# Kernel optimization log

Hardware: AMD Instinct MI355X
Metric: run time of the kernel (lower is better)

The kernel has to match this reference:

```python
import jax, jax.numpy as jnp
import numpy as np

B = 128          # graphs
NPG = 512        # nodes per graph
N = B * NPG      # total nodes
DEG = 8
E = N * DEG      # total edges (intra-graph)
D = 100          # num_feature_dim / num_node_labels
HID = 128        # config.hidden
HEADS = 8
F1 = 20          # per-head dim of first GATConv in each GATNet
RATIO = 0.5
K = int(np.ceil(RATIO * NPG))  # nodes kept per graph by SAGPooling
NEG_SLOPE = 0.2


def setup_inputs() -> dict:
    key = jax.random.key(0)
    ks = jax.random.split(key, 24)
    x = jax.random.randint(ks[0], (N,), 0, D)
    # intra-graph random edges: local ids in [0, NPG) + graph offset
    src_l = jax.random.randint(ks[1], (B, NPG * DEG), 0, NPG)
    dst_l = jax.random.randint(ks[2], (B, NPG * DEG), 0, NPG)
    off = (jnp.arange(B) * NPG)[:, None]
    edge_index = jnp.stack([(src_l + off).ravel(), (dst_l + off).ravel()])
    batch = jnp.repeat(jnp.arange(B), NPG)

    def lin(k, fan_in, fan_out):
        return jax.random.normal(k, (fan_in, fan_out), jnp.float32) / np.sqrt(fan_in)

    def att(k, h, f):
        return jax.random.normal(k, (h, f), jnp.float32) * 0.1

    p = {
        # GATNet A (conv1): GATConv(D, 20, heads=8) then GATConv(160, HID, heads=1)
        "W_a1": lin(ks[3], D, HEADS * F1), "asrc_a1": att(ks[4], HEADS, F1),
        "adst_a1": att(ks[5], HEADS, F1), "b_a1": jnp.zeros((HEADS * F1,), jnp.float32),
        "W_a2": lin(ks[6], HEADS * F1, HID), "asrc_a2": att(ks[7], 1, HID),
        "adst_a2": att(ks[8], 1, HID), "b_a2": jnp.zeros((HID,), jnp.float32),
        # GATNet B (conv4): GATConv(HID, 20, heads=8) then GATConv(160, HID, heads=1)
        "W_b1": lin(ks[9], HID, HEADS * F1), "asrc_b1": att(ks[10], HEADS, F1),
        "adst_b1": att(ks[11], HEADS, F1), "b_b1": jnp.zeros((HEADS * F1,), jnp.float32),
        "W_b2": lin(ks[12], HEADS * F1, HID), "asrc_b2": att(ks[13], 1, HID),
        "adst_b2": att(ks[14], 1, HID), "b_b2": jnp.zeros((HID,), jnp.float32),
        # SAGPooling GraphConv(HID, 1)
        "w_rel": lin(ks[15], HID, 1), "w_root": lin(ks[16], HID, 1),
        "b_pool": jnp.zeros((1,), jnp.float32),
    }
    return {"x": x, "edge_index": edge_index, "batch": batch, **p}


def _gat_conv(h, src, dst, W, asrc, adst, b):
    """PyG GATConv (with self-loops already included in src/dst)."""
    Hh, Ff = asrc.shape
    z = (h @ W).reshape(N, Hh, Ff)                       # [N,H,F]
    es = jnp.sum(z * asrc, axis=-1)                      # [N,H] source logits
    ed = jnp.sum(z * adst, axis=-1)                      # [N,H] dest logits
    e = jax.nn.leaky_relu(es[src] + ed[dst], NEG_SLOPE)  # [E',H]
    m = jax.ops.segment_max(e, dst, num_segments=N)
    m = jnp.where(jnp.isfinite(m), m, 0.0)
    ex = jnp.exp(e - m[dst])
    den = jax.ops.segment_sum(ex, dst, num_segments=N)
    alpha = ex / (den[dst] + 1e-16)
    out = jax.ops.segment_sum(z[src] * alpha[:, :, None], dst, num_segments=N)
    return out.reshape(N, Hh * Ff) + b


def reference(x, edge_index, batch,
              W_a1, asrc_a1, adst_a1, b_a1, W_a2, asrc_a2, adst_a2, b_a2,
              W_b1, asrc_b1, adst_b1, b_b1, W_b2, asrc_b2, adst_b2, b_b2,
              w_rel, w_root, b_pool):
    src, dst = edge_index[0], edge_index[1]
    loops = jnp.arange(N)
    src_sl = jnp.concatenate([src, loops])  # GATConv adds self loops
    dst_sl = jnp.concatenate([dst, loops])

    h = jax.nn.one_hot(x, D, dtype=jnp.float32)
    # GATNet A: conv1 -> relu -> conv2 ; outer relu (dropout is eval no-op)
    h = jax.nn.relu(_gat_conv(h, src_sl, dst_sl, W_a1, asrc_a1, adst_a1, b_a1))
    h = _gat_conv(h, src_sl, dst_sl, W_a2, asrc_a2, adst_a2, b_a2)
    h = jax.nn.relu(h)
    # GATNet B
    h = jax.nn.relu(_gat_conv(h, src_sl, dst_sl, W_b1, asrc_b1, adst_b1, b_b1))
    h = _gat_conv(h, src_sl, dst_sl, W_b2, asrc_b2, adst_b2, b_b2)
    h = jax.nn.relu(h)

    # SAGPooling: GraphConv(HID,1) score (no self loops), tanh, per-graph top-k
    nbr = jax.ops.segment_sum(h[src], dst, num_segments=N)
    score = jnp.tanh(nbr @ w_rel + h @ w_root + b_pool).ravel()   # [N]
    sv, si = jax.lax.top_k(score.reshape(B, NPG), K)              # [B,K]
    perm = (si + (jnp.arange(B) * NPG)[:, None]).ravel()          # global node ids
    x_sel = h[perm] * sv.ravel()[:, None]                         # [B*K, HID]
    pooled = jnp.max(x_sel.reshape(B, K, HID), axis=1)            # global_max_pool
    batch_out = jnp.repeat(jnp.arange(B), K)
    return (pooled, perm, sv.ravel(), batch_out)
```

## Files before the change

kernel.cpp:

```cpp
#include <hip/hip_runtime.h>
#include <math.h>

#define N_NODES 65536
#define NPG     512
#define NGRAPH  128
#define E_EDGES 524288
#define MAXDEG  64
#define NHEADS  8
#define F1      20
#define HID     128
#define D160    160
#define KSEL    256
#define NLBL    100

#define IMG_A2_ELEMS (144*168)
#define IMG_B1_ELEMS (176*136)
#define PB_ZERO 0
#define PB_A2   64
#define PB_B1   (PB_A2 + 95)
#define PB_B2   (PB_B1 + 94)
#define PB_WA1  (PB_B2 + 95)
#define PB_EST  (PB_WA1 + 63)
#define PB_TOT  (PB_EST + 7)

typedef unsigned short ushort_t;
typedef unsigned int   uint_t;
typedef unsigned long long u64;
typedef __attribute__((ext_vector_type(8))) short short8;
typedef __attribute__((ext_vector_type(4))) float f32x4;

__device__ __forceinline__ float lrelu(float x){ return x > 0.f ? x : 0.2f*x; }
__device__ __forceinline__ ushort_t f2bf(float f){
    uint_t u = __float_as_uint(f);
    return (ushort_t)((u + 0x7FFFu + ((u >> 16) & 1u)) >> 16);
}
__device__ __forceinline__ float bf2f(ushort_t u){ return __uint_as_float(((uint_t)u) << 16); }
__device__ __forceinline__ float bflo(uint_t v){ return __uint_as_float(v << 16); }
__device__ __forceinline__ float bfhi(uint_t v){ return __uint_as_float(v & 0xFFFF0000u); }
__device__ __forceinline__ int xswz(int bid, int nblocks){
    return (bid & 7) * (nblocks >> 3) + (bid >> 3);
}

__device__ __forceinline__ u64 comp_make(float s, int idx){
    uint_t u = __float_as_uint(s);
    u ^= (u & 0x80000000u) ? 0xFFFFFFFFu : 0x80000000u;
    return ((u64)u << 32) | (u64)(511 - idx);
}
__device__ __forceinline__ float comp_score(u64 c){
    uint_t u = (uint_t)(c >> 32);
    u ^= (u & 0x80000000u) ? 0x80000000u : 0xFFFFFFFFu;
    return __uint_as_float(u);
}
__device__ __forceinline__ int comp_idx(u64 c){ return 511 - (int)(c & 0x1FFu); }
__device__ __forceinline__ u64 shfl_xor_u64(u64 x, int m){
    uint_t lo = __shfl_xor((uint_t)x, m);
    uint_t hi = __shfl_xor((uint_t)(x >> 32), m);
    return ((u64)hi << 32) | lo;
}

__global__ void k_prep(const float* __restrict__ Wa1, const float* __restrict__ as1,
                       const float* __restrict__ ad1,
                       const float* __restrict__ Wa2, const float* __restrict__ as2,
                       const float* __restrict__ ad2,
                       const float* __restrict__ Wb1, const float* __restrict__ asb1,
                       const float* __restrict__ adb1,
                       const float* __restrict__ Wb2, const float* __restrict__ asb2,
                       const float* __restrict__ adb2,
                       int* __restrict__ deg,
                       ushort_t* __restrict__ imgA2, ushort_t* __restrict__ imgB1,
                       ushort_t* __restrict__ imgB2,
                       ushort_t* __restrict__ Wbf, float* __restrict__ esT,
                       float* __restrict__ edT){
    int bid = blockIdx.x, tid = threadIdx.x;
    if(bid < PB_A2){
        ((uint4*)deg)[(bid - PB_ZERO)*256 + tid] = (uint4){0,0,0,0};
    } else if(bid < PB_B1 || (bid >= PB_B2 && bid < PB_WA1)){
        bool isB2 = (bid >= PB_B2);
        int j = (bid - (isB2 ? PB_B2 : PB_A2))*256 + tid;
        if(j < IMG_A2_ELEMS){
            const float* W  = isB2 ? Wb2 : Wa2;
            const float* as = isB2 ? asb2 : as2;
            const float* ad = isB2 ? adb2 : ad2;
            int n = j / 168, k = j - n*168;
            float v = 0.f;
            if(k < 160){
                if(n < 128) v = W[k*128 + n];
                else if(n < 130){
                    const float* av = (n == 128) ? as : ad;
                    float s = 0.f;
                    for(int c=0; c<128; ++c) s += W[k*128 + c]*av[c];
                    v = s;
                }
            }
            (isB2 ? imgB2 : imgA2)[j] = f2bf(v);
        }
    } else if(bid < PB_B2){
        int j = (bid - PB_B1)*256 + tid;
        if(j < IMG_B1_ELEMS){
            int n = j / 136, k = j - n*136;
            float v = 0.f;
            if(k < 128){
                if(n < 160) v = Wb1[k*160 + n];
                else {
                    int j2 = n - 160, h = j2 & 7;
                    const float* av = ((j2 < 8) ? asb1 : adb1) + h*F1;
                    const float* wr = Wb1 + k*160 + h*F1;
                    float s = 0.f;
                    #pragma unroll
                    for(int f=0; f<F1; ++f) s += wr[f]*av[f];
                    v = s;
                }
            }
            imgB1[j] = f2bf(v);
        }
    } else if(bid < PB_EST){
        int j = (bid - PB_WA1)*256 + tid;
        if(j < NLBL*D160) Wbf[j] = f2bf(Wa1[j]);
    } else {
        int t = (bid - PB_EST)*256 + tid;
        if(t < NLBL*16){
            int lbl = t >> 4, j = t & 15, h = j & 7;
            const float* av = ((j < 8) ? as1 : ad1) + h*F1;
            const float* wr = Wa1 + lbl*D160 + h*F1;
            float s = 0.f;
            #pragma unroll
            for(int f=0; f<F1; ++f) s += wr[f]*av[f];
            if(j < 8) esT[lbl*8 + h] = s;
            else      edT[lbl*8 + h] = s;
        }
    }
}

__global__ void k_build_ell(const int* __restrict__ src, const int* __restrict__ dst,
                            int* __restrict__ deg, int* __restrict__ ell){
    int blk = xswz(blockIdx.x, E_EDGES/256);
    int e = blk*blockDim.x + threadIdx.x;
    int d = dst[e];
    int p = atomicAdd(&deg[d], 1);
    if(p < MAXDEG) ell[d*MAXDEG + p] = src[e];
}

__global__ __launch_bounds__(256) void k_attn8_a(const int* __restrict__ x,
        const int* __restrict__ deg, const int* __restrict__ ell,
        const ushort_t* __restrict__ Wbf, const float* __restrict__ esT,
        const float* __restrict__ edT, const float* __restrict__ bias,
        ushort_t* __restrict__ out){
    __shared__ __align__(16) ushort_t Wl[NLBL*D160];
    __shared__ float esL[NLBL*8], edL[NLBL*8];
    int tid = threadIdx.x;
    for(int i = tid; i < NLBL*D160/8; i += 256)
        ((uint4*)Wl)[i] = ((const uint4*)Wbf)[i];
    for(int i = tid; i < NLBL*8; i += 256){ esL[i] = esT[i]; edL[i] = edT[i]; }
    __syncthreads();
    int blk = xswz(blockIdx.x, N_NODES*NHEADS/256);
    int t = blk*256 + tid;
    int n = t >> 3, h = t & 7;
    int dg = deg[n]; if(dg > MAXDEG) dg = MAXDEG;
    int lbl = x[n];
    float edn = edL[lbl*8 + h];
    float wself = expf(lrelu(esL[lbl*8 + h] + edn));
    float den = wself;
    float acc[F1];
    {
        const uint_t* zn = (const uint_t*)Wl + lbl*80 + h*10;
        #pragma unroll
        for(int f=0; f<10; ++f){
            uint_t v = zn[f];
            acc[2*f]   = wself*bflo(v);
            acc[2*f+1] = wself*bfhi(v);
        }
    }
    const int* el = ell + n*MAXDEG;
    int i = 0;
    for(; i+2 <= dg; i += 2){
        int sa = el[i], sb = el[i+1];
        int la = x[sa], lb = x[sb];
        float wa = expf(lrelu(esL[la*8 + h] + edn));
        float wb = expf(lrelu(esL[lb*8 + h] + edn));
        den += wa + wb;
        const uint_t* za = (const uint_t*)Wl + la*80 + h*10;
        const uint_t* zb = (const uint_t*)Wl + lb*80 + h*10;
        #pragma unroll
        for(int f=0; f<10; ++f){
            uint_t va = za[f], vb = zb[f];
            acc[2*f]   += wa*bflo(va) + wb*bflo(vb);
            acc[2*f+1] += wa*bfhi(va) + wb*bfhi(vb);
        }
    }
    if(i < dg){
        int sa = el[i];
        int la = x[sa];
        float wa = expf(lrelu(esL[la*8 + h] + edn));
        den += wa;
        const uint_t* za = (const uint_t*)Wl + la*80 + h*10;
        #pragma unroll
        for(int f=0; f<10; ++f){
            uint_t va = za[f];
            acc[2*f]   += wa*bflo(va);
            acc[2*f+1] += wa*bfhi(va);
        }
    }
    float inv = 1.f/(den + 1e-16f);
    uint_t* o = (uint_t*)(out + (size_t)n*D160 + h*F1);
    const float* bb = bias + h*F1;
    #pragma unroll
    for(int f=0; f<10; ++f){
        float v0 = fmaxf(acc[2*f]*inv   + bb[2*f],   0.f);
        float v1 = fmaxf(acc[2*f+1]*inv + bb[2*f+1], 0.f);
        o[f] = (uint_t)f2bf(v0) | ((uint_t)f2bf(v1) << 16);
    }
}

__global__ __launch_bounds__(512) void k_attn8b(const int* __restrict__ deg,
        const int* __restrict__ ell, const ushort_t* __restrict__ z8,
        const float* __restrict__ es8, const float* __restrict__ ed8,
        const float* __restrict__ bias, ushort_t* __restrict__ out){
    __shared__ __align__(16) ushort_t zl[512*88];
    __shared__ __align__(16) float4 esl[512];
    __shared__ __align__(16) float4 edl[512];
    int tid = threadIdx.x;
    int blk = xswz(blockIdx.x, NGRAPH*2);
    int g = blk >> 1, hg = blk & 1;
    int base = g*NPG;
    for(int idx = tid; idx < 512*10; idx += 512){
        int row = idx/10, q = idx - (idx/10)*10;
        uint4 v = *(const uint4*)(z8 + (size_t)(base+row)*D160 + hg*80 + q*8);
        *(uint4*)(zl + row*88 + q*8) = v;
    }
    esl[tid] = *(const float4*)(es8 + (size_t)(base+tid)*8 + hg*4);
    edl[tid] = *(const float4*)(ed8 + (size_t)(base+tid)*8 + hg*4);
    __syncthreads();
    int n = tid;
    int dg = deg[base+n]; if(dg > MAXDEG) dg = MAXDEG;
    const int* el = ell + (size_t)(base+n)*MAXDEG;
    float4 edn = edl[n];
    float4 esn = esl[n];
    float w0 = expf(lrelu(esn.x + edn.x));
    float w1 = expf(lrelu(esn.y + edn.y));
    float w2 = expf(lrelu(esn.z + edn.z));
    float w3 = expf(lrelu(esn.w + edn.w));
    float den0 = w0, den1 = w1, den2 = w2, den3 = w3;
    float acc[80];
    #pragma unroll
    for(int q=0; q<10; ++q){
        uint4 v = *(const uint4*)(zl + n*88 + q*8);
        const uint_t* vu = (const uint_t*)&v;
        #pragma unroll
        for(int r=0; r<4; ++r){
            int ch = q*8 + r*2;
            float wA = (ch < 20) ? w0 : (ch < 40) ? w1 : (ch < 60) ? w2 : w3;
            float wB = (ch+1 < 20) ? w0 : (ch+1 < 40) ? w1 : (ch+1 < 60) ? w2 : w3;
            acc[ch]   = wA*bflo(vu[r]);
            acc[ch+1] = wB*bfhi(vu[r]);
        }
    }
    for(int i=0; i<dg; ++i){
        int s = el[i] & (NPG-1);
        float4 es_s = esl[s];
        float wa0 = expf(lrelu(es_s.x + edn.x));
        float wa1 = expf(lrelu(es_s.y + edn.y));
        float wa2 = expf(lrelu(es_s.z + edn.z));
        float wa3 = expf(lrelu(es_s.w + edn.w));
        den0 += wa0; den1 += wa1; den2 += wa2; den3 += wa3;
        #pragma unroll
        for(int q=0; q<10; ++q){
            uint4 v = *(const uint4*)(zl + s*88 + q*8);
            const uint_t* vu = (const uint_t*)&v;
            #pragma unroll
            for(int r=0; r<4; ++r){
                int ch = q*8 + r*2;
                float wA = (ch < 20) ? wa0 : (ch < 40) ? wa1 : (ch < 60) ? wa2 : wa3;
                float wB = (ch+1 < 20) ? wa0 : (ch+1 < 40) ? wa1 : (ch+1 < 60) ? wa2 : wa3;
                acc[ch]   += wA*bflo(vu[r]);
                acc[ch+1] += wB*bfhi(vu[r]);
            }
        }
    }
    float inv0 = 1.f/(den0 + 1e-16f);
    float inv1 = 1.f/(den1 + 1e-16f);
    float inv2 = 1.f/(den2 + 1e-16f);
    float inv3 = 1.f/(den3 + 1e-16f);
    const float* bb = bias + hg*80;
    uint_t* o = (uint_t*)out + (size_t)(base+n)*80 + hg*40;
    #pragma unroll
    for(int q=0; q<10; ++q){
        #pragma unroll
        for(int r=0; r<4; ++r){
            int ch = q*8 + r*2;
            float iA = (ch < 20) ? inv0 : (ch < 40) ? inv1 : (ch < 60) ? inv2 : inv3;
            float iB = (ch+1 < 20) ? inv0 : (ch+1 < 40) ? inv1 : (ch+1 < 60) ? inv2 : inv3;
            float v0 = fmaxf(acc[ch]*iA   + bb[ch],   0.f);
            float v1 = fmaxf(acc[ch+1]*iB + bb[ch+1], 0.f);
            o[q*4 + r] = (uint_t)f2bf(v0) | ((uint_t)f2bf(v1) << 16);
        }
    }
}

template<int IN, int OUTC, int OUTIMG, bool ESED8>
__global__ __launch_bounds__(256) void k_gemm2(const ushort_t* __restrict__ Wimg,
                                               const ushort_t* __restrict__ A,
                                               ushort_t* __restrict__ C,
                                               float* __restrict__ oa,
                                               float* __restrict__ ob){
    constexpr int LDW = IN + 8;
    constexpr int NT = OUTIMG/16;
    constexpr int NC = OUTC/16;
    constexpr int KS = IN/32;
    constexpr int ELEMS = OUTIMG*LDW;
    __shared__ __align__(16) ushort_t Wt[ELEMS];
    int tid = threadIdx.x;
    int blk = xswz(blockIdx.x, N_NODES/64);
    int wave = tid >> 6, lane = tid & 63;
    int col16 = lane & 15;
    int kq = (lane >> 4) * 8;
    int row = blk*64 + wave*16 + col16;
    const ushort_t* Ar = A + (size_t)row*IN + kq;
    short8 afr[KS];
    #pragma unroll
    for(int ks=0; ks<KS; ++ks)
        afr[ks] = *reinterpret_cast<const short8*>(Ar + ks*32);
    for(int i = tid; i < ELEMS/8; i += 256)
        ((uint4*)Wt)[i] = ((const uint4*)Wimg)[i];
    __syncthreads();
    f32x4 acc[NT];
    #pragma unroll
    for(int c=0;c<NT;++c) acc[c] = (f32x4){0.f,0.f,0.f,0.f};
    #pragma unroll
    for(int ks=0; ks<KS; ++ks){
        #pragma unroll
        for(int c=0;c<NT;++c){
            short8 bf = *reinterpret_cast<const short8*>(&Wt[(c*16 + col16)*LDW + ks*32 + kq]);
            acc[c] = __builtin_amdgcn_mfma_f32_16x16x32_bf16(afr[ks], bf, acc[c], 0, 0, 0);
        }
    }
    int rbase = blk*64 + wave*16 + (lane >> 4)*4;
    #pragma unroll
    for(int c=0;c<NC;++c){
        #pragma unroll
        for(int r=0;r<4;++r){
            C[(size_t)(rbase + r)*OUTC + c*16 + col16] = f2bf(acc[c][r]);
        }
    }
    if(ESED8){
        #pragma unroll
        for(int r=0;r<4;++r){
            float v = acc[NT-1][r];
            if(col16 < 8) oa[(size_t)(rbase + r)*8 + col16] = v;
            else          ob[(size_t)(rbase + r)*8 + (col16 - 8)] = v;
        }
    } else {
        if(col16 == 0){
            #pragma unroll
            for(int r=0;r<4;++r) oa[rbase + r] = acc[NT-1][r];
        }
        if(col16 == 1){
            #pragma unroll
            for(int r=0;r<4;++r) ob[rbase + r] = acc[NT-1][r];
        }
    }
}

template<bool DOT>
__global__ void k_attn1v(const int* __restrict__ deg, const int* __restrict__ ell,
                         const ushort_t* __restrict__ Z, const float* __restrict__ es,
                         const float* __restrict__ ed, const float* __restrict__ bias,
                         ushort_t* __restrict__ out,
                         const float* __restrict__ wa, const float* __restrict__ wb,
                         float* __restrict__ oa, float* __restrict__ ob){
    int blk = xswz(blockIdx.x, N_NODES*4/256);
    int t = blk*256 + threadIdx.x;
    int n = t >> 2, qt = t & 3;
    int dg = deg[n]; if(dg > MAXDEG) dg = MAXDEG;
    float edn = ed[n];
    float wself = expf(lrelu(es[n] + edn));
    float den = wself;
    const uint4* Zu = (const uint4*)Z;
    float acc[32];
    {
        const uint4* zr = Zu + (size_t)n*16 + qt*4;
        uint4 vs[4];
        #pragma unroll
        for(int q=0;q<4;++q) vs[q] = zr[q];
        #pragma unroll
        for(int q=0;q<4;++q){
            const uint_t* vu = (const uint_t*)&vs[q];
            #pragma unroll
            for(int r=0;r<4;++r){
                acc[q*8+r*2]   = wself*bflo(vu[r]);
                acc[q*8+r*2+1] = wself*bfhi(vu[r]);
            }
        }
    }
    const int* el = ell + (size_t)n*MAXDEG;
    int i = 0;
    for(; i+2 <= dg; i += 2){
        int sa = el[i], sb = el[i+1];
        float ea = es[sa], eb = es[sb];
        const uint4* za = Zu + (size_t)sa*16 + qt*4;
        const uint4* zb = Zu + (size_t)sb*16 + qt*4;
        uint4 va[4], vb4[4];
        #pragma unroll
        for(int q=0;q<4;++q){ va[q] = za[q]; vb4[q] = zb[q]; }
        float wA = expf(lrelu(ea + edn));
        float wB = expf(lrelu(eb + edn));
        den += wA + wB;
        #pragma unroll
        for(int q=0;q<4;++q){
            const uint_t* au = (const uint_t*)&va[q];
            const uint_t* bu = (const uint_t*)&vb4[q];
            #pragma unroll
            for(int r=0;r<4;++r){
                acc[q*8+r*2]   += wA*bflo(au[r]) + wB*bflo(bu[r]);
                acc[q*8+r*2+1] += wA*bfhi(au[r]) + wB*bfhi(bu[r]);
            }
        }
    }
    if(i < dg){
        int sa = el[i];
        float ea = es[sa];
        const uint4* za = Zu + (size_t)sa*16 + qt*4;
        uint4 va[4];
        #pragma unroll
        for(int q=0;q<4;++q) va[q] = za[q];
        float wA = expf(lrelu(ea + edn));
        den += wA;
        #pragma unroll
        for(int q=0;q<4;++q){
            const uint_t* au = (const uint_t*)&va[q];
            #pragma unroll
            for(int r=0;r<4;++r){
                acc[q*8+r*2]   += wA*bflo(au[r]);
                acc[q*8+r*2+1] += wA*bfhi(au[r]);
            }
        }
    }
    float inv = 1.f/(den + 1e-16f);
    const float* bb = bias + qt*32;
    float pa = 0.f, pb = 0.f;
    uint_t* o = (uint_t*)out + (size_t)n*64 + qt*16;
    #pragma unroll
    for(int q=0;q<4;++q){
        uint4 w;
        uint_t* wu = (uint_t*)&w;
        #pragma unroll
        for(int r=0;r<4;++r){
            int ch = q*8 + r*2;
            float r0 = fmaxf(acc[ch]*inv   + bb[ch],   0.f);
            float r1 = fmaxf(acc[ch+1]*inv + bb[ch+1], 0.f);
            wu[r] = (uint_t)f2bf(r0) | ((uint_t)f2bf(r1) << 16);
            if(DOT){
                pa += r0*wa[qt*32 + ch] + r1*wa[qt*32 + ch + 1];
                pb += r0*wb[qt*32 + ch] + r1*wb[qt*32 + ch + 1];
            }
        }
        *(uint4*)(o + q*4) = w;
    }
    if(DOT){
        pa += __shfl_xor(pa, 1); pa += __shfl_xor(pa, 2);
        pb += __shfl_xor(pb, 1); pb += __shfl_xor(pb, 2);
        if(qt == 0){ oa[n] = pa; ob[n] = pb; }
    }
}

__global__ void k_score(const int* __restrict__ deg, const int* __restrict__ ell,
                        const float* __restrict__ yrel, const float* __restrict__ rroot,
                        const float* __restrict__ bpool, float* __restrict__ score){
    int blk = xswz(blockIdx.x, N_NODES/256);
    int n = blk*blockDim.x + threadIdx.x;
    int dg = deg[n]; if(dg > MAXDEG) dg = MAXDEG;
    float s = rroot[n] + bpool[0];
    const int* el = ell + n*MAXDEG;
    int i = 0;
    for(; i+4 <= dg; i += 4){
        float y0 = yrel[el[i]],   y1 = yrel[el[i+1]];
        float y2 = yrel[el[i+2]], y3 = yrel[el[i+3]];
        s += (y0 + y1) + (y2 + y3);
    }
    for(; i < dg; ++i) s += yrel[el[i]];
    score[n] = tanhf(s);
}

__global__ __launch_bounds__(512) void k_topk_pool(const float* __restrict__ score,
                                                   const ushort_t* __restrict__ H,
                                                   float* __restrict__ pooled,
                                                   float* __restrict__ perm_f,
                                                   float* __restrict__ sv,
                                                   float* __restrict__ batch_f){
    __shared__ int   sidx[KSEL];
    __shared__ float sval[KSEL];
    __shared__ float pmax[512];
    int g = xswz(blockIdx.x, NGRAPH);
    int base = g*NPG;
    int t = threadIdx.x;
    if(t < 64){
        int l = t;
        u64 v[8];
        #pragma unroll
        for(int r=0;r<8;++r){
            int i = r*64 + l;
            v[r] = comp_make(score[base + i], i);
        }
        #pragma unroll
        for(int kk=1; kk<=9; ++kk){
            int k = 1 << kk;
            #pragma unroll
            for(int jj=kk-1; jj>=0; --jj){
                int j = 1 << jj;
                if(j < 64){
                    bool lower = (l & j) == 0;
                    #pragma unroll
                    for(int r=0;r<8;++r){
                        int i = r*64 + l;
                        u64 p = shfl_xor_u64(v[r], j);
                        bool desc = (i & k) == 0;
                        u64 mx = v[r] > p ? v[r] : p;
                        u64 mn = v[r] > p ? p : v[r];
                        v[r] = (lower == desc) ? mx : mn;
                    }
                } else {
                    int jr = j >> 6;
                    #pragma unroll
                    for(int r=0;r<8;++r){
                        if((r & jr) == 0){
                            int rp = r | jr;
                            int i = r*64 + l;
                            bool desc = (i & k) == 0;
                            u64 a = v[r], b = v[rp];
                            u64 mx = a > b ? a : b;
                            u64 mn = a > b ? b : a;
                            v[r]  = desc ? mx : mn;
                            v[rp] = desc ? mn : mx;
                        }
                    }
                }
            }
        }
        #pragma unroll
        for(int r=0;r<4;++r){
            int i = r*64 + l;
            int idx = comp_idx(v[r]);
            float s = comp_score(v[r]);
            perm_f[g*KSEL + i]  = (float)(base + idx);
            sv[g*KSEL + i]      = s;
            batch_f[g*KSEL + i] = (float)g;
            sidx[i] = idx; sval[i] = s;
        }
    }
    __syncthreads();
    int c = t & 127, kc = t >> 7;
    float mx = -1e30f;
    for(int kk = kc*64; kk < kc*64 + 64; ++kk){
        mx = fmaxf(mx, bf2f(H[(size_t)(base + sidx[kk])*HID + c]) * sval[kk]);
    }
    pmax[t] = mx;
    __syncthreads();
    if(t < HID){
        pooled[g*HID + t] = fmaxf(fmaxf(pmax[t], pmax[t+128]),
                                  fmaxf(pmax[t+256], pmax[t+384]));
    }
}

extern "C" void kernel_launch(void* const* d_in, const int* in_sizes, int n_in,
                              void* d_out, int out_size, void* d_ws, size_t ws_size,
                              hipStream_t stream) {
    const int*   x       = (const int*)  d_in[0];
    const int*   eidx    = (const int*)  d_in[1];
    const float* W_a1    = (const float*)d_in[3];
    const float* asrc_a1 = (const float*)d_in[4];
    const float* adst_a1 = (const float*)d_in[5];
    const float* b_a1    = (const float*)d_in[6];
    const float* W_a2    = (const float*)d_in[7];
    const float* asrc_a2 = (const float*)d_in[8];
    const float* adst_a2 = (const float*)d_in[9];
    const float* b_a2    = (const float*)d_in[10];
    const float* W_b1    = (const float*)d_in[11];
    const float* asrc_b1 = (const float*)d_in[12];
    const float* adst_b1 = (const float*)d_in[13];
    const float* b_b1    = (const float*)d_in[14];
    const float* W_b2    = (const float*)d_in[15];
    const float* asrc_b2 = (const float*)d_in[16];
    const float* adst_b2 = (const float*)d_in[17];
    const float* b_b2    = (const float*)d_in[18];
    const float* w_rel   = (const float*)d_in[19];
    const float* w_root  = (const float*)d_in[20];
    const float* b_pool  = (const float*)d_in[21];

    const int* e_src = eidx;
    const int* e_dst = eidx + E_EDGES;

    char* ws = (char*)d_ws;
    size_t off = 0;
    auto alloc = [&](size_t bytes)->char*{
        char* p = ws + off;
        off += (bytes + 255) & ~(size_t)255;
        return p;
    };
    int*      deg    = (int*)     alloc((size_t)N_NODES*4);
    int*      ell    = (int*)     alloc((size_t)N_NODES*MAXDEG*4);
    ushort_t* z8     = (ushort_t*)alloc((size_t)N_NODES*D160*2);
    ushort_t* h8     = (ushort_t*)alloc((size_t)N_NODES*D160*2);
    ushort_t* zc     = (ushort_t*)alloc((size_t)N_NODES*HID*2);
    ushort_t* hmid   = (ushort_t*)alloc((size_t)N_NODES*HID*2);
    ushort_t* hfin   = (ushort_t*)alloc((size_t)N_NODES*HID*2);
    float*    es8    = (float*)   alloc((size_t)N_NODES*NHEADS*4);
    float*    ed8    = (float*)   alloc((size_t)N_NODES*NHEADS*4);
    float*    es1    = (float*)   alloc((size_t)N_NODES*4);
    float*    ed1    = (float*)   alloc((size_t)N_NODES*4);
    float*    yrel   = (float*)   alloc((size_t)N_NODES*4);
    float*    rroot  = (float*)   alloc((size_t)N_NODES*4);
    float*    score  = (float*)   alloc((size_t)N_NODES*4);
    ushort_t* Wbf    = (ushort_t*)alloc((size_t)NLBL*D160*2);
    float*    esT    = (float*)   alloc((size_t)NLBL*8*4);
    float*    edT    = (float*)   alloc((size_t)NLBL*8*4);
    ushort_t* imgA2  = (ushort_t*)alloc((size_t)IMG_A2_ELEMS*2);
    ushort_t* imgB1  = (ushort_t*)alloc((size_t)IMG_B1_ELEMS*2);
    ushort_t* imgB2  = (ushort_t*)alloc((size_t)IMG_A2_ELEMS*2);
    (void)ws_size; (void)n_in; (void)in_sizes; (void)out_size;

    float* out      = (float*)d_out;
    float* pooled   = out;
    float* perm_f   = out + NGRAPH*HID;
    float* sv       = perm_f + NGRAPH*KSEL;
    float* batch_f  = sv + NGRAPH*KSEL;

    k_prep<<<PB_TOT, 256, 0, stream>>>(W_a1, asrc_a1, adst_a1,
                                       W_a2, asrc_a2, adst_a2,
                                       W_b1, asrc_b1, adst_b1,
                                       W_b2, asrc_b2, adst_b2,
                                       deg, imgA2, imgB1, imgB2, Wbf, esT, edT);
    k_build_ell<<<E_EDGES/256, 256, 0, stream>>>(e_src, e_dst, deg, ell);

    k_attn8_a<<<N_NODES*NHEADS/256, 256, 0, stream>>>(x, deg, ell, Wbf, esT, edT, b_a1, h8);

    k_gemm2<D160, HID, 144, false><<<N_NODES/64, 256, 0, stream>>>(imgA2, h8, zc, es1, ed1);
    k_attn1v<false><<<N_NODES*4/256, 256, 0, stream>>>(deg, ell, zc, es1, ed1, b_a2, hmid,
                                                       nullptr, nullptr, nullptr, nullptr);

    k_gemm2<HID, D160, 176, true><<<N_NODES/64, 256, 0, stream>>>(imgB1, hmid, z8, es8, ed8);
    k_attn8b<<<NGRAPH*2, 512, 0, stream>>>(deg, ell, z8, es8, ed8, b_b1, h8);

    k_gemm2<D160, HID, 144, false><<<N_NODES/64, 256, 0, stream>>>(imgB2, h8, zc, es1, ed1);
    k_attn1v<true><<<N_NODES*4/256, 256, 0, stream>>>(deg, ell, zc, es1, ed1, b_b2, hfin,
                                                      w_rel, w_root, yrel, rroot);

    k_score<<<N_NODES/256, 256, 0, stream>>>(deg, ell, yrel, rroot, b_pool, score);
    k_topk_pool<<<NGRAPH, NPG, 0, stream>>>(score, hfin, pooled, perm_f, sv, batch_f);
}
```

Before: 226.5 us.

## Sort nodes by in-degree per graph to balance warp work in aggregation kernels

Adds a per-graph counting-sort kernel that orders nodes by in-degree and builds a permutation. The four neighbour-aggregation kernels and the score kernel now map threads to nodes through this permutation, so each wavefront handles nodes of similar degree and spends fewer lanes idle in the variable-length neighbour loops. The cost is an extra small kernel launch plus an indirect node lookup. Output writes become scattered and less coalesced.

```diff
diff --git a/kernel.cpp b/kernel.cpp
--- a/kernel.cpp
+++ b/kernel.cpp
@@ -140,8 +140,30 @@
     if(p < MAXDEG) ell[d*MAXDEG + p] = src[e];
 }
 
+__global__ __launch_bounds__(512) void k_degsort(const int* __restrict__ deg,
+                                                 int* __restrict__ perm){
+    __shared__ int hist[MAXDEG+1];
+    __shared__ int bofs[MAXDEG+1];
+    int g = blockIdx.x;
+    int base = g*NPG;
+    int t = threadIdx.x;
+    if(t <= MAXDEG) hist[t] = 0;
+    __syncthreads();
+    int d = deg[base + t]; if(d > MAXDEG) d = MAXDEG;
+    atomicAdd(&hist[d], 1);
+    __syncthreads();
+    if(t == 0){
+        int run = 0;
+        for(int b = 0; b <= MAXDEG; ++b){ bofs[b] = run; run += hist[b]; }
+    }
+    __syncthreads();
+    int pos = atomicAdd(&bofs[d], 1);
+    perm[base + pos] = base + t;
+}
+
 __global__ __launch_bounds__(256) void k_attn8_a(const int* __restrict__ x,
         const int* __restrict__ deg, const int* __restrict__ ell,
+        const int* __restrict__ perm,
         const ushort_t* __restrict__ Wbf, const float* __restrict__ esT,
         const float* __restrict__ edT, const float* __restrict__ bias,
         ushort_t* __restrict__ out){
@@ -154,7 +176,7 @@
     __syncthreads();
     int blk = xswz(blockIdx.x, N_NODES*NHEADS/256);
     int t = blk*256 + tid;
-    int n = t >> 3, h = t & 7;
+    int n = perm[t >> 3], h = t & 7;
     int dg = deg[n]; if(dg > MAXDEG) dg = MAXDEG;
     int lbl = x[n];
     float edn = edL[lbl*8 + h];
@@ -170,7 +192,7 @@
             acc[2*f+1] = wself*bfhi(v);
         }
     }
-    const int* el = ell + n*MAXDEG;
+    const int* el = ell + (size_t)n*MAXDEG;
     int i = 0;
     for(; i+2 <= dg; i += 2){
         int sa = el[i], sb = el[i+1];
@@ -212,7 +234,8 @@
 }
 
 __global__ __launch_bounds__(512) void k_attn8b(const int* __restrict__ deg,
-        const int* __restrict__ ell, const ushort_t* __restrict__ z8,
+        const int* __restrict__ ell, const int* __restrict__ perm,
+        const ushort_t* __restrict__ z8,
         const float* __restrict__ es8, const float* __restrict__ ed8,
         const float* __restrict__ bias, ushort_t* __restrict__ out){
     __shared__ __align__(16) ushort_t zl[512*88];
@@ -230,7 +253,7 @@
     esl[tid] = *(const float4*)(es8 + (size_t)(base+tid)*8 + hg*4);
     edl[tid] = *(const float4*)(ed8 + (size_t)(base+tid)*8 + hg*4);
     __syncthreads();
-    int n = tid;
+    int n = perm[base + tid] - base;
     int dg = deg[base+n]; if(dg > MAXDEG) dg = MAXDEG;
     const int* el = ell + (size_t)(base+n)*MAXDEG;
     float4 edn = edl[n];
@@ -362,6 +385,7 @@
 
 template<bool DOT>
 __global__ void k_attn1v(const int* __restrict__ deg, const int* __restrict__ ell,
+                         const int* __restrict__ perm,
                          const ushort_t* __restrict__ Z, const float* __restrict__ es,
                          const float* __restrict__ ed, const float* __restrict__ bias,
                          ushort_t* __restrict__ out,
@@ -369,7 +393,7 @@
                          float* __restrict__ oa, float* __restrict__ ob){
     int blk = xswz(blockIdx.x, N_NODES*4/256);
     int t = blk*256 + threadIdx.x;
-    int n = t >> 2, qt = t & 3;
+    int n = perm[t >> 2], qt = t & 3;
     int dg = deg[n]; if(dg > MAXDEG) dg = MAXDEG;
     float edn = ed[n];
     float wself = expf(lrelu(es[n] + edn));
@@ -463,13 +487,14 @@
 }
 
 __global__ void k_score(const int* __restrict__ deg, const int* __restrict__ ell,
+                        const int* __restrict__ perm,
                         const float* __restrict__ yrel, const float* __restrict__ rroot,
                         const float* __restrict__ bpool, float* __restrict__ score){
     int blk = xswz(blockIdx.x, N_NODES/256);
-    int n = blk*blockDim.x + threadIdx.x;
+    int n = perm[blk*blockDim.x + threadIdx.x];
     int dg = deg[n]; if(dg > MAXDEG) dg = MAXDEG;
     float s = rroot[n] + bpool[0];
-    const int* el = ell + n*MAXDEG;
+    const int* el = ell + (size_t)n*MAXDEG;
     int i = 0;
     for(; i+4 <= dg; i += 4){
         float y0 = yrel[el[i]],   y1 = yrel[el[i+1]];
@@ -597,6 +622,7 @@
     };
     int*      deg    = (int*)     alloc((size_t)N_NODES*4);
     int*      ell    = (int*)     alloc((size_t)N_NODES*MAXDEG*4);
+    int*      nperm  = (int*)     alloc((size_t)N_NODES*4);
     ushort_t* z8     = (ushort_t*)alloc((size_t)N_NODES*D160*2);
     ushort_t* h8     = (ushort_t*)alloc((size_t)N_NODES*D160*2);
     ushort_t* zc     = (ushort_t*)alloc((size_t)N_NODES*HID*2);
@@ -629,20 +655,21 @@
                                        W_b2, asrc_b2, adst_b2,
                                        deg, imgA2, imgB1, imgB2, Wbf, esT, edT);
     k_build_ell<<<E_EDGES/256, 256, 0, stream>>>(e_src, e_dst, deg, ell);
-
-    k_attn8_a<<<N_NODES*NHEADS/256, 256, 0, stream>>>(x, deg, ell, Wbf, esT, edT, b_a1, h8);
+    k_degsort<<<NGRAPH, NPG, 0, stream>>>(deg, nperm);
+
+    k_attn8_a<<<N_NODES*NHEADS/256, 256, 0, stream>>>(x, deg, ell, nperm, Wbf, esT, edT, b_a1, h8);
 
     k_gemm2<D160, HID, 144, false><<<N_NODES/64, 256, 0, stream>>>(imgA2, h8, zc, es1, ed1);
-    k_attn1v<false><<<N_NODES*4/256, 256, 0, stream>>>(deg, ell, zc, es1, ed1, b_a2, hmid,
+    k_attn1v<false><<<N_NODES*4/256, 256, 0, stream>>>(deg, ell, nperm, zc, es1, ed1, b_a2, hmid,
                                                        nullptr, nullptr, nullptr, nullptr);
 
     k_gemm2<HID, D160, 176, true><<<N_NODES/64, 256, 0, stream>>>(imgB1, hmid, z8, es8, ed8);
-    k_attn8b<<<NGRAPH*2, 512, 0, stream>>>(deg, ell, z8, es8, ed8, b_b1, h8);
+    k_attn8b<<<NGRAPH*2, 512, 0, stream>>>(deg, ell, nperm, z8, es8, ed8, b_b1, h8);
 
     k_gemm2<D160, HID, 144, false><<<N_NODES/64, 256, 0, stream>>>(imgB2, h8, zc, es1, ed1);
-    k_attn1v<true><<<N_NODES*4/256, 256, 0, stream>>>(deg, ell, zc, es1, ed1, b_b2, hfin,
+    k_attn1v<true><<<N_NODES*4/256, 256, 0, stream>>>(deg, ell, nperm, zc, es1, ed1, b_b2, hfin,
                                                       w_rel, w_root, yrel, rroot);
 
-    k_score<<<N_NODES/256, 256, 0, stream>>>(deg, ell, yrel, rroot, b_pool, score);
+    k_score<<<N_NODES/256, 256, 0, stream>>>(deg, ell, nperm, yrel, rroot, b_pool, score);
     k_topk_pool<<<NGRAPH, NPG, 0, stream>>>(score, hfin, pooled, perm_f, sv, batch_f);
 }
```

After: 228.4 us. Within noise of the previous version (+0.8%).
